# Kernel tuning notes

Measured on AMD Instinct MI355X. Metric: run time of the kernel, lower is better.

## Reference

```python
import jax, jax.numpy as jnp
import numpy as np

N_WIRES = 12
DIM = 1 << N_WIRES  # 4096
BSZ = 1024


def _cnot_ring_perm(n):
    """Composed permutation for CNOT(i, (i+1)%n) applied for i=0..n-1.
    Wire 0 is the most significant bit (torchquantum convention: state
    reshaped [bsz, 2, 2, ..., 2] with dim 1 = wire 0).
    out_state[j] = in_state[perm[j]].
    """
    idx = np.arange(1 << n, dtype=np.int64)
    gates = [(i, (i + 1) % n) for i in range(n)]
    # s_final[j] = s0[p_1(p_2(...p_K(j)))] -> apply gates in reverse order
    for c, t in reversed(gates):
        cbit = (idx >> (n - 1 - c)) & 1
        idx = idx ^ (cbit << (n - 1 - t))
    return jnp.asarray(idx, dtype=jnp.int32)


_PERM = _cnot_ring_perm(N_WIRES)


def setup_inputs() -> dict:
    key = jax.random.key(0)
    k0, k1, k2, k3, k4 = jax.random.split(key, 5)
    scale = 1.0 / np.sqrt(DIM)
    return {
        "x": jax.random.normal(k0, (BSZ, DIM), dtype=jnp.float32),
        "U_re": jax.random.normal(k1, (DIM, DIM), dtype=jnp.float32) * scale,
        "U_im": jax.random.normal(k2, (DIM, DIM), dtype=jnp.float32) * scale,
        "U1_re": jax.random.normal(k3, (DIM, DIM), dtype=jnp.float32) * scale,
        "U1_im": jax.random.normal(k4, (DIM, DIM), dtype=jnp.float32) * scale,
    }


def reference(x, U_re, U_im, U1_re, U1_im):
    # StateEncoder: L2-normalize each row -> complex statevector [bsz, 2^n]
    norm = jnp.linalg.norm(x, axis=-1, keepdims=True)
    state = (x / norm).astype(jnp.complex64)

    # TrainableUnitary over all wires: state <- U @ state
    U = U_re + 1j * U_im
    state = jnp.einsum("ij,bj->bi", U, state)

    # Ring of CNOTs: precomposed static amplitude permutation
    state = state[:, _PERM]

    # Second trainable unitary
    U1 = U1_re + 1j * U1_im
    state = jnp.einsum("ij,bj->bi", U1, state)

    # |amplitude| per basis state
    return jnp.abs(state)
```

## Files before the change

kernel.cpp:

```cpp
#include <hip/hip_runtime.h>
#include <stdint.h>
#include <math.h>

#define NW   12
#define DIM  4096
#define BSZ  1024

typedef short s16x8 __attribute__((ext_vector_type(8)));
typedef float f32x16 __attribute__((ext_vector_type(16)));

__device__ __forceinline__ ushort f2bf(float x) {
    uint32_t u = __float_as_uint(x);
    uint32_t r = u + 0x7FFFu + ((u >> 16) & 1u);
    return (ushort)(r >> 16);
}
__device__ __forceinline__ float bf2f(ushort h) {
    return __uint_as_float(((uint32_t)h) << 16);
}
__device__ __forceinline__ void split2(float x, ushort& h, ushort& l) {
    h = f2bf(x);
    l = f2bf(x - bf2f(h));
}

__device__ __forceinline__ int perm12(int j) {
    int idx = j;
#pragma unroll
    for (int g = NW - 1; g >= 0; --g) {
        const int c = g;
        const int t = (g + 1) % NW;
        const int cbit = (idx >> (NW - 1 - c)) & 1;
        idx ^= cbit << (NW - 1 - t);
    }
    return idx;
}

__global__ void perm_kernel(int* __restrict__ invp) {
    const int j = blockIdx.x * blockDim.x + threadIdx.x;
    if (j < DIM) invp[perm12(j)] = j;
}

__global__ __launch_bounds__(256) void norm_split_kernel(const float* __restrict__ X,
                                                         ushort* __restrict__ Xh,
                                                         ushort* __restrict__ Xl) {
    const int b = blockIdx.x;
    const float* row = X + (size_t)b * DIM;
    float s = 0.f;
    for (int i = threadIdx.x; i < DIM; i += 256) {
        const float v = row[i];
        s += v * v;
    }
#pragma unroll
    for (int off = 32; off > 0; off >>= 1) s += __shfl_down(s, off, 64);
    __shared__ float ws4[4];
    if ((threadIdx.x & 63) == 0) ws4[threadIdx.x >> 6] = s;
    __syncthreads();
    const float inv = 1.0f / sqrtf(ws4[0] + ws4[1] + ws4[2] + ws4[3]);

    const float4* X4 = (const float4*)row;
#pragma unroll
    for (int j = 0; j < 4; ++j) {
        const int c = j * 256 + threadIdx.x;
        float4 v = X4[c];
        ushort h0, l0, h1, l1, h2, l2, h3, l3;
        split2(v.x * inv, h0, l0);
        split2(v.y * inv, h1, l1);
        split2(v.z * inv, h2, l2);
        split2(v.w * inv, h3, l3);
        uint2 hp, lp;
        hp.x = (uint)h0 | ((uint)h1 << 16); hp.y = (uint)h2 | ((uint)h3 << 16);
        lp.x = (uint)l0 | ((uint)l1 << 16); lp.y = (uint)l2 | ((uint)l3 << 16);
        *(uint2*)(Xh + (size_t)b * DIM + c * 4) = hp;
        *(uint2*)(Xl + (size_t)b * DIM + c * 4) = lp;
    }
}

__global__ __launch_bounds__(256, 2) void stage1(
    const ushort* __restrict__ Xh, const ushort* __restrict__ Xl,
    const float* __restrict__ Ure, const float* __restrict__ Uim,
    const int* __restrict__ invp,
    ushort* __restrict__ Srh, ushort* __restrict__ Srl,
    ushort* __restrict__ Sih, ushort* __restrict__ Sil) {
    __shared__ short Ah[4][128][8], Al[4][128][8];
    __shared__ short Bh0[4][64][8], Bl0[4][64][8];
    __shared__ short Bh1[4][64][8], Bl1[4][64][8];

    const int t    = threadIdx.x;
    const int lane = t & 63;
    const int w    = t >> 6;
    const int wm   = w >> 1, wn = w & 1;
    const int bn   = blockIdx.x * 64;
    const int bm   = blockIdx.y * 128;

    uint4  pAh[2], pAl[2];
    float4 pBr[2], pBi[2];

#define S1_LOAD(k0)                                                         \
    {                                                                       \
        _Pragma("unroll") for (int j = 0; j < 2; ++j) {                     \
            const int ch = j * 256 + t;                                     \
            const int ar = ch >> 2, akb = ch & 3;                           \
            const size_t ga = (size_t)(bm + ar) * DIM + (k0) + akb * 8;     \
            pAh[j] = *(const uint4*)(Xh + ga);                              \
            pAl[j] = *(const uint4*)(Xl + ga);                              \
            const int br = ch >> 3, fc = ch & 7;                            \
            const size_t gb = (size_t)(bn + br) * DIM + (k0) + fc * 4;      \
            pBr[j] = *(const float4*)(Ure + gb);                            \
            pBi[j] = *(const float4*)(Uim + gb);                            \
        }                                                                   \
    }

    f32x16 accr[2], acci[2];
#pragma unroll
    for (int mi = 0; mi < 2; ++mi)
#pragma unroll
        for (int e = 0; e < 16; ++e) { accr[mi][e] = 0.f; acci[mi][e] = 0.f; }

    S1_LOAD(0);

    for (int k0 = 0; k0 < DIM; k0 += 32) {
        __syncthreads();
#pragma unroll
        for (int j = 0; j < 2; ++j) {
            const int ch = j * 256 + t;
            const int ar = ch >> 2, akb = ch & 3;
            *(uint4*)&Ah[akb][ar][0] = pAh[j];
            *(uint4*)&Al[akb][ar][0] = pAl[j];
            const int br = ch >> 3, fc = ch & 7;
            const int bkb = fc >> 1, bo = (fc & 1) * 4;
            ushort h0, l0, h1, l1, h2, l2, h3, l3;
            split2(pBr[j].x, h0, l0); split2(pBr[j].y, h1, l1);
            split2(pBr[j].z, h2, l2); split2(pBr[j].w, h3, l3);
            *(uint2*)&Bh0[bkb][br][bo] = make_uint2((uint)h0 | ((uint)h1 << 16), (uint)h2 | ((uint)h3 << 16));
            *(uint2*)&Bl0[bkb][br][bo] = make_uint2((uint)l0 | ((uint)l1 << 16), (uint)l2 | ((uint)l3 << 16));
            split2(pBi[j].x, h0, l0); split2(pBi[j].y, h1, l1);
            split2(pBi[j].z, h2, l2); split2(pBi[j].w, h3, l3);
            *(uint2*)&Bh1[bkb][br][bo] = make_uint2((uint)h0 | ((uint)h1 << 16), (uint)h2 | ((uint)h3 << 16));
            *(uint2*)&Bl1[bkb][br][bo] = make_uint2((uint)l0 | ((uint)l1 << 16), (uint)l2 | ((uint)l3 << 16));
        }
        __syncthreads();
        if (k0 + 32 < DIM) S1_LOAD(k0 + 32);

#pragma unroll
        for (int ks = 0; ks < 2; ++ks) {
            const int kb = ks * 2 + (lane >> 5);
            const int r  = lane & 31;
            const s16x8 bh0 = *(const s16x8*)&Bh0[kb][wn * 32 + r][0];
            const s16x8 bl0 = *(const s16x8*)&Bl0[kb][wn * 32 + r][0];
            const s16x8 bh1 = *(const s16x8*)&Bh1[kb][wn * 32 + r][0];
            const s16x8 bl1 = *(const s16x8*)&Bl1[kb][wn * 32 + r][0];
#pragma unroll
            for (int mi = 0; mi < 2; ++mi) {
                const s16x8 ah = *(const s16x8*)&Ah[kb][wm * 64 + mi * 32 + r][0];
                const s16x8 al = *(const s16x8*)&Al[kb][wm * 64 + mi * 32 + r][0];
                accr[mi] = __builtin_amdgcn_mfma_f32_32x32x16_bf16(ah, bh0, accr[mi], 0, 0, 0);
                accr[mi] = __builtin_amdgcn_mfma_f32_32x32x16_bf16(al, bh0, accr[mi], 0, 0, 0);
                accr[mi] = __builtin_amdgcn_mfma_f32_32x32x16_bf16(ah, bl0, accr[mi], 0, 0, 0);
                acci[mi] = __builtin_amdgcn_mfma_f32_32x32x16_bf16(ah, bh1, acci[mi], 0, 0, 0);
                acci[mi] = __builtin_amdgcn_mfma_f32_32x32x16_bf16(al, bh1, acci[mi], 0, 0, 0);
                acci[mi] = __builtin_amdgcn_mfma_f32_32x32x16_bf16(ah, bl1, acci[mi], 0, 0, 0);
            }
        }
    }

    const int col = bn + wn * 32 + (lane & 31);
    const int pc  = invp[col];
#pragma unroll
    for (int mi = 0; mi < 2; ++mi) {
#pragma unroll
        for (int reg = 0; reg < 16; ++reg) {
            const int rl   = (reg & 3) + 8 * (reg >> 2) + 4 * (lane >> 5);
            const int grow = bm + wm * 64 + mi * 32 + rl;
            const size_t o = (size_t)grow * DIM + pc;
            ushort h, l;
            split2(accr[mi][reg], h, l);
            Srh[o] = h; Srl[o] = l;
            split2(acci[mi][reg], h, l);
            Sih[o] = h; Sil[o] = l;
        }
    }
#undef S1_LOAD
}

__global__ __launch_bounds__(256, 2) void stage2(
    const ushort* __restrict__ Srh, const ushort* __restrict__ Srl,
    const ushort* __restrict__ Sih, const ushort* __restrict__ Sil,
    const float* __restrict__ U1re, const float* __restrict__ U1im,
    float* __restrict__ Out) {
    __shared__ short Arh[4][128][8], Arl[4][128][8];
    __shared__ short Aih[4][128][8], Ail[4][128][8];
    __shared__ short Bh0[4][64][8], Bl0[4][64][8];
    __shared__ short Bh1[4][64][8], Bl1[4][64][8];

    const int t    = threadIdx.x;
    const int lane = t & 63;
    const int w    = t >> 6;
    const int wm   = w >> 1, wn = w & 1;
    const int bn   = blockIdx.x * 64;
    const int bm   = blockIdx.y * 128;

    uint4  pRh[2], pRl[2], pIh[2], pIl[2];
    float4 pBr[2], pBi[2];

#define S2_LOAD(k0)                                                         \
    {                                                                       \
        _Pragma("unroll") for (int j = 0; j < 2; ++j) {                     \
            const int ch = j * 256 + t;                                     \
            const int ar = ch >> 2, akb = ch & 3;                           \
            const size_t ga = (size_t)(bm + ar) * DIM + (k0) + akb * 8;     \
            pRh[j] = *(const uint4*)(Srh + ga);                             \
            pRl[j] = *(const uint4*)(Srl + ga);                             \
            pIh[j] = *(const uint4*)(Sih + ga);                             \
            pIl[j] = *(const uint4*)(Sil + ga);                             \
            const int br = ch >> 3, fc = ch & 7;                            \
            const size_t gb = (size_t)(bn + br) * DIM + (k0) + fc * 4;      \
            pBr[j] = *(const float4*)(U1re + gb);                           \
            pBi[j] = *(const float4*)(U1im + gb);                           \
        }                                                                   \
    }

    f32x16 accr[2], acci[2];
#pragma unroll
    for (int mi = 0; mi < 2; ++mi)
#pragma unroll
        for (int e = 0; e < 16; ++e) { accr[mi][e] = 0.f; acci[mi][e] = 0.f; }

    S2_LOAD(0);

    for (int k0 = 0; k0 < DIM; k0 += 32) {
        __syncthreads();
#pragma unroll
        for (int j = 0; j < 2; ++j) {
            const int ch = j * 256 + t;
            const int ar = ch >> 2, akb = ch & 3;
            *(uint4*)&Arh[akb][ar][0] = pRh[j];
            *(uint4*)&Arl[akb][ar][0] = pRl[j];
            *(uint4*)&Aih[akb][ar][0] = pIh[j];
            *(uint4*)&Ail[akb][ar][0] = pIl[j];
            const int br = ch >> 3, fc = ch & 7;
            const int bkb = fc >> 1, bo = (fc & 1) * 4;
            ushort h0, l0, h1, l1, h2, l2, h3, l3;
            split2(pBr[j].x, h0, l0); split2(pBr[j].y, h1, l1);
            split2(pBr[j].z, h2, l2); split2(pBr[j].w, h3, l3);
            *(uint2*)&Bh0[bkb][br][bo] = make_uint2((uint)h0 | ((uint)h1 << 16), (uint)h2 | ((uint)h3 << 16));
            *(uint2*)&Bl0[bkb][br][bo] = make_uint2((uint)l0 | ((uint)l1 << 16), (uint)l2 | ((uint)l3 << 16));
            split2(pBi[j].x, h0, l0); split2(pBi[j].y, h1, l1);
            split2(pBi[j].z, h2, l2); split2(pBi[j].w, h3, l3);
            *(uint2*)&Bh1[bkb][br][bo] = make_uint2((uint)h0 | ((uint)h1 << 16), (uint)h2 | ((uint)h3 << 16));
            *(uint2*)&Bl1[bkb][br][bo] = make_uint2((uint)l0 | ((uint)l1 << 16), (uint)l2 | ((uint)l3 << 16));
        }
        __syncthreads();
        if (k0 + 32 < DIM) S2_LOAD(k0 + 32);

#pragma unroll
        for (int ks = 0; ks < 2; ++ks) {
            const int kb = ks * 2 + (lane >> 5);
            const int r  = lane & 31;
            const s16x8 urh = *(const s16x8*)&Bh0[kb][wn * 32 + r][0];
            const s16x8 url = *(const s16x8*)&Bl0[kb][wn * 32 + r][0];
            const s16x8 uih = *(const s16x8*)&Bh1[kb][wn * 32 + r][0];
            const s16x8 uil = *(const s16x8*)&Bl1[kb][wn * 32 + r][0];
            const s16x8 nuih = uih ^ (short)0x8000;
            const s16x8 nuil = uil ^ (short)0x8000;
#pragma unroll
            for (int mi = 0; mi < 2; ++mi) {
                const int arow = wm * 64 + mi * 32 + r;
                const s16x8 srh = *(const s16x8*)&Arh[kb][arow][0];
                const s16x8 srl = *(const s16x8*)&Arl[kb][arow][0];
                const s16x8 sih = *(const s16x8*)&Aih[kb][arow][0];
                const s16x8 sil = *(const s16x8*)&Ail[kb][arow][0];
                accr[mi] = __builtin_amdgcn_mfma_f32_32x32x16_bf16(srh, urh,  accr[mi], 0, 0, 0);
                accr[mi] = __builtin_amdgcn_mfma_f32_32x32x16_bf16(srl, urh,  accr[mi], 0, 0, 0);
                accr[mi] = __builtin_amdgcn_mfma_f32_32x32x16_bf16(srh, url,  accr[mi], 0, 0, 0);
                accr[mi] = __builtin_amdgcn_mfma_f32_32x32x16_bf16(sih, nuih, accr[mi], 0, 0, 0);
                accr[mi] = __builtin_amdgcn_mfma_f32_32x32x16_bf16(sil, nuih, accr[mi], 0, 0, 0);
                accr[mi] = __builtin_amdgcn_mfma_f32_32x32x16_bf16(sih, nuil, accr[mi], 0, 0, 0);
                acci[mi] = __builtin_amdgcn_mfma_f32_32x32x16_bf16(srh, uih,  acci[mi], 0, 0, 0);
                acci[mi] = __builtin_amdgcn_mfma_f32_32x32x16_bf16(srl, uih,  acci[mi], 0, 0, 0);
                acci[mi] = __builtin_amdgcn_mfma_f32_32x32x16_bf16(srh, uil,  acci[mi], 0, 0, 0);
                acci[mi] = __builtin_amdgcn_mfma_f32_32x32x16_bf16(sih, urh,  acci[mi], 0, 0, 0);
                acci[mi] = __builtin_amdgcn_mfma_f32_32x32x16_bf16(sil, urh,  acci[mi], 0, 0, 0);
                acci[mi] = __builtin_amdgcn_mfma_f32_32x32x16_bf16(sih, url,  acci[mi], 0, 0, 0);
            }
        }
    }

    const int col = bn + wn * 32 + (lane & 31);
#pragma unroll
    for (int mi = 0; mi < 2; ++mi) {
#pragma unroll
        for (int reg = 0; reg < 16; ++reg) {
            const int rl   = (reg & 3) + 8 * (reg >> 2) + 4 * (lane >> 5);
            const int grow = bm + wm * 64 + mi * 32 + rl;
            const float vr = accr[mi][reg], vi = acci[mi][reg];
            Out[(size_t)grow * DIM + col] = sqrtf(vr * vr + vi * vi);
        }
    }
#undef S2_LOAD
}

extern "C" void kernel_launch(void* const* d_in, const int* in_sizes, int n_in,
                              void* d_out, int out_size, void* d_ws, size_t ws_size,
                              hipStream_t stream) {
    const float* X    = (const float*)d_in[0];
    const float* Ure  = (const float*)d_in[1];
    const float* Uim  = (const float*)d_in[2];
    const float* U1re = (const float*)d_in[3];
    const float* U1im = (const float*)d_in[4];
    float* Out = (float*)d_out;

    char* w = (char*)d_ws;
    const size_t MAT = (size_t)BSZ * DIM;
    int*    invp = (int*)w;
    ushort* Xh   = (ushort*)(w + (1 << 14));
    ushort* Xl   = Xh + MAT;
    ushort* Srh  = Xl + MAT;
    ushort* Srl  = Srh + MAT;
    ushort* Sih  = Srl + MAT;
    ushort* Sil  = Sih + MAT;

    perm_kernel<<<DIM / 256, 256, 0, stream>>>(invp);
    norm_split_kernel<<<BSZ, 256, 0, stream>>>(X, Xh, Xl);

    dim3 grid(DIM / 64, BSZ / 128);
    stage1<<<grid, 256, 0, stream>>>(Xh, Xl, Ure, Uim, invp, Srh, Srl, Sih, Sil);
    stage2<<<grid, 256, 0, stream>>>(Srh, Srl, Sih, Sil, U1re, U1im, Out);
}
```

Baseline: 1.487 ms.

## Presplit unitaries to bf16 hi/lo and stream tiles via global_load_lds

Adds presplit kernels that convert U and U1 into bf16 hi/lo planes once per call, folding the CNOT permutation into U1's columns so stage1 can write its output unpermuted. The GEMM stages then copy tiles straight from global memory into LDS with global_load_lds, dropping the in-loop float-to-bf16 split, register staging and scattered stores. The grid is transposed so blocks sharing a U column tile run together for L2 reuse. The cost is extra workspace, two extra passes over the 4096x4096 matrices, and the loss of the register prefetch that overlapped loads with MFMA work; a fallback keeps the old path when workspace is too small.

```diff
diff --git a/kernel.cpp b/kernel.cpp
--- a/kernel.cpp
+++ b/kernel.cpp
@@ -21,6 +21,14 @@
     h = f2bf(x);
     l = f2bf(x - bf2f(h));
 }
+__device__ __forceinline__ uint pack2(ushort a, ushort b) {
+    return (uint)a | ((uint)b << 16);
+}
+
+#define GL16(G, L)                                                            \
+    __builtin_amdgcn_global_load_lds(                                         \
+        (const __attribute__((address_space(1))) unsigned int*)(const void*)(G), \
+        (__attribute__((address_space(3))) unsigned int*)(void*)(L), 16, 0, 0)
 
 __device__ __forceinline__ int perm12(int j) {
     int idx = j;
@@ -66,15 +74,219 @@
         split2(v.y * inv, h1, l1);
         split2(v.z * inv, h2, l2);
         split2(v.w * inv, h3, l3);
-        uint2 hp, lp;
-        hp.x = (uint)h0 | ((uint)h1 << 16); hp.y = (uint)h2 | ((uint)h3 << 16);
-        lp.x = (uint)l0 | ((uint)l1 << 16); lp.y = (uint)l2 | ((uint)l3 << 16);
-        *(uint2*)(Xh + (size_t)b * DIM + c * 4) = hp;
-        *(uint2*)(Xl + (size_t)b * DIM + c * 4) = lp;
-    }
-}
-
-__global__ __launch_bounds__(256, 2) void stage1(
+        *(uint2*)(Xh + (size_t)b * DIM + c * 4) = make_uint2(pack2(h0, h1), pack2(h2, h3));
+        *(uint2*)(Xl + (size_t)b * DIM + c * 4) = make_uint2(pack2(l0, l1), pack2(l2, l3));
+    }
+}
+
+template <bool PERM>
+__global__ __launch_bounds__(256) void presplit(
+    const float* __restrict__ Re, const float* __restrict__ Im,
+    const int* __restrict__ gidx,
+    ushort* __restrict__ Rh, ushort* __restrict__ Rl,
+    ushort* __restrict__ Ih, ushort* __restrict__ Il) {
+    const size_t base = (size_t)blockIdx.x * DIM;
+#pragma unroll
+    for (int c = 0; c < 4; ++c) {
+        const int col = c * 1024 + threadIdx.x * 4;
+        float vr[4], vi[4];
+        if constexpr (PERM) {
+            const int4 g = *(const int4*)&gidx[col];
+            vr[0] = Re[base + g.x]; vr[1] = Re[base + g.y];
+            vr[2] = Re[base + g.z]; vr[3] = Re[base + g.w];
+            vi[0] = Im[base + g.x]; vi[1] = Im[base + g.y];
+            vi[2] = Im[base + g.z]; vi[3] = Im[base + g.w];
+        } else {
+            const float4 a = *(const float4*)&Re[base + col];
+            const float4 b = *(const float4*)&Im[base + col];
+            vr[0] = a.x; vr[1] = a.y; vr[2] = a.z; vr[3] = a.w;
+            vi[0] = b.x; vi[1] = b.y; vi[2] = b.z; vi[3] = b.w;
+        }
+        ushort h0, l0, h1, l1, h2, l2, h3, l3;
+        split2(vr[0], h0, l0); split2(vr[1], h1, l1);
+        split2(vr[2], h2, l2); split2(vr[3], h3, l3);
+        *(uint2*)&Rh[base + col] = make_uint2(pack2(h0, h1), pack2(h2, h3));
+        *(uint2*)&Rl[base + col] = make_uint2(pack2(l0, l1), pack2(l2, l3));
+        split2(vi[0], h0, l0); split2(vi[1], h1, l1);
+        split2(vi[2], h2, l2); split2(vi[3], h3, l3);
+        *(uint2*)&Ih[base + col] = make_uint2(pack2(h0, h1), pack2(h2, h3));
+        *(uint2*)&Il[base + col] = make_uint2(pack2(l0, l1), pack2(l2, l3));
+    }
+}
+
+__global__ __launch_bounds__(256, 2) void stage1_gl(
+    const ushort* __restrict__ Xh, const ushort* __restrict__ Xl,
+    const ushort* __restrict__ Urh, const ushort* __restrict__ Url,
+    const ushort* __restrict__ Uih, const ushort* __restrict__ Uil,
+    ushort* __restrict__ Srh, ushort* __restrict__ Srl,
+    ushort* __restrict__ Sih, ushort* __restrict__ Sil) {
+    __shared__ short Ab[2][4][128][8];
+    __shared__ short Bb[4][4][64][8];
+
+    const int t = threadIdx.x, lane = t & 63, w = t >> 6;
+    const int wm = w >> 1, wn = w & 1;
+    const int bm = blockIdx.x * 128;
+    const int bn = blockIdx.y * 64;
+
+    const ushort* Amat[2] = {Xh, Xl};
+    const ushort* Bmat[4] = {Urh, Url, Uih, Uil};
+    const ushort* gsrc[8];
+    short* ldst[8];
+#pragma unroll
+    for (int q = 0; q < 8; ++q) {
+        const int g = w * 8 + q;
+        if (g < 16) {
+            const int mat = g >> 3, kb = (g >> 1) & 3, half = g & 1;
+            gsrc[q] = Amat[mat] + (size_t)(bm + half * 64 + lane) * DIM + kb * 8;
+            ldst[q] = &Ab[mat][kb][half * 64][0];
+        } else {
+            const int h = g - 16, mat = h >> 2, kb = h & 3;
+            gsrc[q] = Bmat[mat] + (size_t)(bn + lane) * DIM + kb * 8;
+            ldst[q] = &Bb[mat][kb][0][0];
+        }
+    }
+
+    f32x16 accr[2], acci[2];
+#pragma unroll
+    for (int mi = 0; mi < 2; ++mi)
+#pragma unroll
+        for (int e = 0; e < 16; ++e) { accr[mi][e] = 0.f; acci[mi][e] = 0.f; }
+
+    for (int k0 = 0; k0 < DIM; k0 += 32) {
+#pragma unroll
+        for (int q = 0; q < 8; ++q) GL16(gsrc[q] + k0, ldst[q]);
+        __syncthreads();
+#pragma unroll
+        for (int ks = 0; ks < 2; ++ks) {
+            const int kb = ks * 2 + (lane >> 5);
+            const int r  = lane & 31;
+            const s16x8 urh = *(const s16x8*)&Bb[0][kb][wn * 32 + r][0];
+            const s16x8 url = *(const s16x8*)&Bb[1][kb][wn * 32 + r][0];
+            const s16x8 uih = *(const s16x8*)&Bb[2][kb][wn * 32 + r][0];
+            const s16x8 uil = *(const s16x8*)&Bb[3][kb][wn * 32 + r][0];
+#pragma unroll
+            for (int mi = 0; mi < 2; ++mi) {
+                const int ar = wm * 64 + mi * 32 + r;
+                const s16x8 ah = *(const s16x8*)&Ab[0][kb][ar][0];
+                const s16x8 al = *(const s16x8*)&Ab[1][kb][ar][0];
+                accr[mi] = __builtin_amdgcn_mfma_f32_32x32x16_bf16(ah, urh, accr[mi], 0, 0, 0);
+                accr[mi] = __builtin_amdgcn_mfma_f32_32x32x16_bf16(al, urh, accr[mi], 0, 0, 0);
+                accr[mi] = __builtin_amdgcn_mfma_f32_32x32x16_bf16(ah, url, accr[mi], 0, 0, 0);
+                acci[mi] = __builtin_amdgcn_mfma_f32_32x32x16_bf16(ah, uih, acci[mi], 0, 0, 0);
+                acci[mi] = __builtin_amdgcn_mfma_f32_32x32x16_bf16(al, uih, acci[mi], 0, 0, 0);
+                acci[mi] = __builtin_amdgcn_mfma_f32_32x32x16_bf16(ah, uil, acci[mi], 0, 0, 0);
+            }
+        }
+        __syncthreads();
+    }
+
+    const int col = bn + wn * 32 + (lane & 31);
+#pragma unroll
+    for (int mi = 0; mi < 2; ++mi) {
+#pragma unroll
+        for (int reg = 0; reg < 16; ++reg) {
+            const int rl  = (reg & 3) + 8 * (reg >> 2) + 4 * (lane >> 5);
+            const int row = bm + wm * 64 + mi * 32 + rl;
+            const size_t o = (size_t)row * DIM + col;
+            ushort h, l;
+            split2(accr[mi][reg], h, l);
+            Srh[o] = h; Srl[o] = l;
+            split2(acci[mi][reg], h, l);
+            Sih[o] = h; Sil[o] = l;
+        }
+    }
+}
+
+__global__ __launch_bounds__(256, 2) void stage2_gl(
+    const ushort* __restrict__ Srh, const ushort* __restrict__ Srl,
+    const ushort* __restrict__ Sih, const ushort* __restrict__ Sil,
+    const ushort* __restrict__ Vrh, const ushort* __restrict__ Vrl,
+    const ushort* __restrict__ Vih, const ushort* __restrict__ Vil,
+    float* __restrict__ Out) {
+    __shared__ short Ab[4][4][128][8];
+    __shared__ short Bb[4][4][64][8];
+
+    const int t = threadIdx.x, lane = t & 63, w = t >> 6;
+    const int wm = w >> 1, wn = w & 1;
+    const int bm = blockIdx.x * 128;
+    const int bn = blockIdx.y * 64;
+
+    const ushort* Amat[4] = {Srh, Srl, Sih, Sil};
+    const ushort* Bmat[4] = {Vrh, Vrl, Vih, Vil};
+    const ushort* gsrc[12];
+    short* ldst[12];
+#pragma unroll
+    for (int q = 0; q < 12; ++q) {
+        const int g = w * 12 + q;
+        if (g < 32) {
+            const int mat = g >> 3, kb = (g >> 1) & 3, half = g & 1;
+            gsrc[q] = Amat[mat] + (size_t)(bm + half * 64 + lane) * DIM + kb * 8;
+            ldst[q] = &Ab[mat][kb][half * 64][0];
+        } else {
+            const int h = g - 32, mat = h >> 2, kb = h & 3;
+            gsrc[q] = Bmat[mat] + (size_t)(bn + lane) * DIM + kb * 8;
+            ldst[q] = &Bb[mat][kb][0][0];
+        }
+    }
+
+    f32x16 accr[2], acci[2];
+#pragma unroll
+    for (int mi = 0; mi < 2; ++mi)
+#pragma unroll
+        for (int e = 0; e < 16; ++e) { accr[mi][e] = 0.f; acci[mi][e] = 0.f; }
+
+    for (int k0 = 0; k0 < DIM; k0 += 32) {
+#pragma unroll
+        for (int q = 0; q < 12; ++q) GL16(gsrc[q] + k0, ldst[q]);
+        __syncthreads();
+#pragma unroll
+        for (int ks = 0; ks < 2; ++ks) {
+            const int kb = ks * 2 + (lane >> 5);
+            const int r  = lane & 31;
+            const s16x8 urh = *(const s16x8*)&Bb[0][kb][wn * 32 + r][0];
+            const s16x8 url = *(const s16x8*)&Bb[1][kb][wn * 32 + r][0];
+            const s16x8 uih = *(const s16x8*)&Bb[2][kb][wn * 32 + r][0];
+            const s16x8 uil = *(const s16x8*)&Bb[3][kb][wn * 32 + r][0];
+            const s16x8 nuih = uih ^ (short)0x8000;
+            const s16x8 nuil = uil ^ (short)0x8000;
+#pragma unroll
+            for (int mi = 0; mi < 2; ++mi) {
+                const int ar = wm * 64 + mi * 32 + r;
+                const s16x8 srh = *(const s16x8*)&Ab[0][kb][ar][0];
+                const s16x8 srl = *(const s16x8*)&Ab[1][kb][ar][0];
+                const s16x8 sih = *(const s16x8*)&Ab[2][kb][ar][0];
+                const s16x8 sil = *(const s16x8*)&Ab[3][kb][ar][0];
+                accr[mi] = __builtin_amdgcn_mfma_f32_32x32x16_bf16(srh, urh,  accr[mi], 0, 0, 0);
+                accr[mi] = __builtin_amdgcn_mfma_f32_32x32x16_bf16(srl, urh,  accr[mi], 0, 0, 0);
+                accr[mi] = __builtin_amdgcn_mfma_f32_32x32x16_bf16(srh, url,  accr[mi], 0, 0, 0);
+                accr[mi] = __builtin_amdgcn_mfma_f32_32x32x16_bf16(sih, nuih, accr[mi], 0, 0, 0);
+                accr[mi] = __builtin_amdgcn_mfma_f32_32x32x16_bf16(sil, nuih, accr[mi], 0, 0, 0);
+                accr[mi] = __builtin_amdgcn_mfma_f32_32x32x16_bf16(sih, nuil, accr[mi], 0, 0, 0);
+                acci[mi] = __builtin_amdgcn_mfma_f32_32x32x16_bf16(srh, uih,  acci[mi], 0, 0, 0);
+                acci[mi] = __builtin_amdgcn_mfma_f32_32x32x16_bf16(srl, uih,  acci[mi], 0, 0, 0);
+                acci[mi] = __builtin_amdgcn_mfma_f32_32x32x16_bf16(srh, uil,  acci[mi], 0, 0, 0);
+                acci[mi] = __builtin_amdgcn_mfma_f32_32x32x16_bf16(sih, urh,  acci[mi], 0, 0, 0);
+                acci[mi] = __builtin_amdgcn_mfma_f32_32x32x16_bf16(sil, urh,  acci[mi], 0, 0, 0);
+                acci[mi] = __builtin_amdgcn_mfma_f32_32x32x16_bf16(sih, url,  acci[mi], 0, 0, 0);
+            }
+        }
+        __syncthreads();
+    }
+
+    const int col = bn + wn * 32 + (lane & 31);
+#pragma unroll
+    for (int mi = 0; mi < 2; ++mi) {
+#pragma unroll
+        for (int reg = 0; reg < 16; ++reg) {
+            const int rl  = (reg & 3) + 8 * (reg >> 2) + 4 * (lane >> 5);
+            const int row = bm + wm * 64 + mi * 32 + rl;
+            const float vr = accr[mi][reg], vi = acci[mi][reg];
+            Out[(size_t)row * DIM + col] = sqrtf(vr * vr + vi * vi);
+        }
+    }
+}
+
+__global__ __launch_bounds__(256, 2) void stage1_fb(
     const ushort* __restrict__ Xh, const ushort* __restrict__ Xl,
     const float* __restrict__ Ure, const float* __restrict__ Uim,
     const int* __restrict__ invp,
@@ -84,14 +296,14 @@
     __shared__ short Bh0[4][64][8], Bl0[4][64][8];
     __shared__ short Bh1[4][64][8], Bl1[4][64][8];
 
-    const int t    = threadIdx.x;
+    const int t = threadIdx.x;
     const int lane = t & 63;
-    const int w    = t >> 6;
-    const int wm   = w >> 1, wn = w & 1;
-    const int bn   = blockIdx.x * 64;
-    const int bm   = blockIdx.y * 128;
-
-    uint4  pAh[2], pAl[2];
+    const int w = t >> 6;
+    const int wm = w >> 1, wn = w & 1;
+    const int bn = blockIdx.x * 64;
+    const int bm = blockIdx.y * 128;
+
+    uint4 pAh[2], pAl[2];
     float4 pBr[2], pBi[2];
 
 #define S1_LOAD(k0)                                                         \
@@ -130,12 +342,12 @@
             ushort h0, l0, h1, l1, h2, l2, h3, l3;
             split2(pBr[j].x, h0, l0); split2(pBr[j].y, h1, l1);
             split2(pBr[j].z, h2, l2); split2(pBr[j].w, h3, l3);
-            *(uint2*)&Bh0[bkb][br][bo] = make_uint2((uint)h0 | ((uint)h1 << 16), (uint)h2 | ((uint)h3 << 16));
-            *(uint2*)&Bl0[bkb][br][bo] = make_uint2((uint)l0 | ((uint)l1 << 16), (uint)l2 | ((uint)l3 << 16));
+            *(uint2*)&Bh0[bkb][br][bo] = make_uint2(pack2(h0, h1), pack2(h2, h3));
+            *(uint2*)&Bl0[bkb][br][bo] = make_uint2(pack2(l0, l1), pack2(l2, l3));
             split2(pBi[j].x, h0, l0); split2(pBi[j].y, h1, l1);
             split2(pBi[j].z, h2, l2); split2(pBi[j].w, h3, l3);
-            *(uint2*)&Bh1[bkb][br][bo] = make_uint2((uint)h0 | ((uint)h1 << 16), (uint)h2 | ((uint)h3 << 16));
-            *(uint2*)&Bl1[bkb][br][bo] = make_uint2((uint)l0 | ((uint)l1 << 16), (uint)l2 | ((uint)l3 << 16));
+            *(uint2*)&Bh1[bkb][br][bo] = make_uint2(pack2(h0, h1), pack2(h2, h3));
+            *(uint2*)&Bl1[bkb][br][bo] = make_uint2(pack2(l0, l1), pack2(l2, l3));
         }
         __syncthreads();
         if (k0 + 32 < DIM) S1_LOAD(k0 + 32);
@@ -181,7 +393,7 @@
 #undef S1_LOAD
 }
 
-__global__ __launch_bounds__(256, 2) void stage2(
+__global__ __launch_bounds__(256, 2) void stage2_fb(
     const ushort* __restrict__ Srh, const ushort* __restrict__ Srl,
     const ushort* __restrict__ Sih, const ushort* __restrict__ Sil,
     const float* __restrict__ U1re, const float* __restrict__ U1im,
@@ -191,14 +403,14 @@
     __shared__ short Bh0[4][64][8], Bl0[4][64][8];
     __shared__ short Bh1[4][64][8], Bl1[4][64][8];
 
-    const int t    = threadIdx.x;
+    const int t = threadIdx.x;
     const int lane = t & 63;
-    const int w    = t >> 6;
-    const int wm   = w >> 1, wn = w & 1;
-    const int bn   = blockIdx.x * 64;
-    const int bm   = blockIdx.y * 128;
-
-    uint4  pRh[2], pRl[2], pIh[2], pIl[2];
+    const int w = t >> 6;
+    const int wm = w >> 1, wn = w & 1;
+    const int bn = blockIdx.x * 64;
+    const int bm = blockIdx.y * 128;
+
+    uint4 pRh[2], pRl[2], pIh[2], pIl[2];
     float4 pBr[2], pBi[2];
 
 #define S2_LOAD(k0)                                                         \
@@ -241,12 +453,12 @@
             ushort h0, l0, h1, l1, h2, l2, h3, l3;
             split2(pBr[j].x, h0, l0); split2(pBr[j].y, h1, l1);
             split2(pBr[j].z, h2, l2); split2(pBr[j].w, h3, l3);
-            *(uint2*)&Bh0[bkb][br][bo] = make_uint2((uint)h0 | ((uint)h1 << 16), (uint)h2 | ((uint)h3 << 16));
-            *(uint2*)&Bl0[bkb][br][bo] = make_uint2((uint)l0 | ((uint)l1 << 16), (uint)l2 | ((uint)l3 << 16));
+            *(uint2*)&Bh0[bkb][br][bo] = make_uint2(pack2(h0, h1), pack2(h2, h3));
+            *(uint2*)&Bl0[bkb][br][bo] = make_uint2(pack2(l0, l1), pack2(l2, l3));
             split2(pBi[j].x, h0, l0); split2(pBi[j].y, h1, l1);
             split2(pBi[j].z, h2, l2); split2(pBi[j].w, h3, l3);
-            *(uint2*)&Bh1[bkb][br][bo] = make_uint2((uint)h0 | ((uint)h1 << 16), (uint)h2 | ((uint)h3 << 16));
-            *(uint2*)&Bl1[bkb][br][bo] = make_uint2((uint)l0 | ((uint)l1 << 16), (uint)l2 | ((uint)l3 << 16));
+            *(uint2*)&Bh1[bkb][br][bo] = make_uint2(pack2(h0, h1), pack2(h2, h3));
+            *(uint2*)&Bl1[bkb][br][bo] = make_uint2(pack2(l0, l1), pack2(l2, l3));
         }
         __syncthreads();
         if (k0 + 32 < DIM) S2_LOAD(k0 + 32);
@@ -308,20 +520,55 @@
     const float* U1im = (const float*)d_in[4];
     float* Out = (float*)d_out;
 
-    char* w = (char*)d_ws;
-    const size_t MAT = (size_t)BSZ * DIM;
-    int*    invp = (int*)w;
-    ushort* Xh   = (ushort*)(w + (1 << 14));
-    ushort* Xl   = Xh + MAT;
-    ushort* Srh  = Xl + MAT;
-    ushort* Srl  = Srh + MAT;
-    ushort* Sih  = Srl + MAT;
-    ushort* Sil  = Sih + MAT;
-
-    perm_kernel<<<DIM / 256, 256, 0, stream>>>(invp);
-    norm_split_kernel<<<BSZ, 256, 0, stream>>>(X, Xh, Xl);
-
-    dim3 grid(DIM / 64, BSZ / 128);
-    stage1<<<grid, 256, 0, stream>>>(Xh, Xl, Ure, Uim, invp, Srh, Srl, Sih, Sil);
-    stage2<<<grid, 256, 0, stream>>>(Srh, Srl, Sih, Sil, U1re, U1im, Out);
-}
+    char* wsp = (char*)d_ws;
+    const size_t MATX = (size_t)BSZ * DIM;
+    const size_t MATU = (size_t)DIM * DIM;
+    const size_t NEED = 16384 + 6 * MATX * 2 + 8 * MATU * 2;
+
+    int* invp = (int*)wsp;
+
+    if (ws_size >= NEED) {
+        char* p = wsp + 16384;
+        ushort* Xh  = (ushort*)p; p += MATX * 2;
+        ushort* Xl  = (ushort*)p; p += MATX * 2;
+        ushort* Srh = (ushort*)p; p += MATX * 2;
+        ushort* Srl = (ushort*)p; p += MATX * 2;
+        ushort* Sih = (ushort*)p; p += MATX * 2;
+        ushort* Sil = (ushort*)p; p += MATX * 2;
+        ushort* Urh = (ushort*)p; p += MATU * 2;
+        ushort* Url = (ushort*)p; p += MATU * 2;
+        ushort* Uih = (ushort*)p; p += MATU * 2;
+        ushort* Uil = (ushort*)p; p += MATU * 2;
+        ushort* Vrh = (ushort*)p; p += MATU * 2;
+        ushort* Vrl = (ushort*)p; p += MATU * 2;
+        ushort* Vih = (ushort*)p; p += MATU * 2;
+        ushort* Vil = (ushort*)p; p += MATU * 2;
+
+        perm_kernel<<<DIM / 256, 256, 0, stream>>>(invp);
+        norm_split_kernel<<<BSZ, 256, 0, stream>>>(X, Xh, Xl);
+        presplit<false><<<DIM, 256, 0, stream>>>(Ure, Uim, invp, Urh, Url, Uih, Uil);
+        presplit<true><<<DIM, 256, 0, stream>>>(U1re, U1im, invp, Vrh, Vrl, Vih, Vil);
+
+        dim3 grid(BSZ / 128, DIM / 64);
+        stage1_gl<<<grid, 256, 0, stream>>>(Xh, Xl, Urh, Url, Uih, Uil,
+                                            Srh, Srl, Sih, Sil);
+        stage2_gl<<<grid, 256, 0, stream>>>(Srh, Srl, Sih, Sil,
+                                            Vrh, Vrl, Vih, Vil, Out);
+    } else {
+        char* p = wsp + 16384;
+        ushort* Xh  = (ushort*)p; p += MATX * 2;
+        ushort* Xl  = (ushort*)p; p += MATX * 2;
+        ushort* Srh = (ushort*)p; p += MATX * 2;
+        ushort* Srl = (ushort*)p; p += MATX * 2;
+        ushort* Sih = (ushort*)p; p += MATX * 2;
+        ushort* Sil = (ushort*)p; p += MATX * 2;
+
+        perm_kernel<<<DIM / 256, 256, 0, stream>>>(invp);
+        norm_split_kernel<<<BSZ, 256, 0, stream>>>(X, Xh, Xl);
+
+        dim3 grid(DIM / 64, BSZ / 128);
+        stage1_fb<<<grid, 256, 0, stream>>>(Xh, Xl, Ure, Uim, invp,
+                                            Srh, Srl, Sih, Sil);
+        stage2_fb<<<grid, 256, 0, stream>>>(Srh, Srl, Sih, Sil, U1re, U1im, Out);
+    }
+}
```

After: 1.485 ms. About the same (-0.1%).
